# Performance work log

Hardware: AMD Instinct MI355X
Metric: run time of the kernel (lower is better)

The kernel has to match this reference:

```python
import jax, jax.numpy as jnp
import numpy as np


def setup_inputs() -> dict:
    key = jax.random.key(0)
    k1, k2 = jax.random.split(key)
    bz, c, h, w = 8, 512, 64, 64
    x = jax.random.normal(k1, (bz, c, h, w), dtype=jnp.float32)
    # binary mask over spatial positions; flag is its flattened view (must be consistent)
    mask = jax.random.randint(k2, (h, w), 0, 2, dtype=jnp.int32)
    flag = mask.reshape(-1)
    return {"input": x, "mask": mask, "flag": flag,
            "shift_sz": 1, "stride": 1, "triple_w": 1}


def reference(input, mask, flag, shift_sz, stride, triple_w):
    # input: [B, C, H, W]; former = first C/2 channels (decoder feats),
    # latter = last C/2 channels (encoder feats). shift_sz=stride=1 -> 1x1 patches,
    # i.e. per-pixel feature vectors.
    bz, c, h, w = input.shape
    ch = c // 2
    S = h * w
    former = input[:, :ch]                      # [B, ch, H, W]
    latter = input[:, ch:]                      # [B, ch, H, W]

    f = former.reshape(bz, ch, S).transpose(0, 2, 1)   # [B, S, ch] query pixels
    l = latter.reshape(bz, ch, S).transpose(0, 2, 1)   # [B, S, ch] key pixels

    # _norm: L2-normalize latter patches (rows)
    l_norm = l / jnp.maximum(jnp.linalg.norm(l, axis=-1, keepdims=True), 1e-12)

    # cosine-style similarity between every former pixel and every latter pixel
    sim = jnp.einsum('bqc,bkc->bqk', f, l_norm)        # [B, S, S]

    # only non-masked (flag==0) latter pixels are valid match candidates
    neg = jnp.asarray(-1e30, sim.dtype)
    sim = jnp.where((flag == 0)[None, None, :], sim, neg)
    idx = jnp.argmax(sim, axis=-1)                     # [B, S] nearest-neighbor index

    # gather matched latter pixels; paste only at masked (flag==1) positions,
    # zero elsewhere (masked_fill_(inv_ex_mask, 0) zeroes the non-mask region)
    shifted = jnp.take_along_axis(l, idx[..., None], axis=1)       # [B, S, ch]
    shifted = jnp.where((flag == 1)[None, :, None], shifted, 0.0)
    shifted = shifted.transpose(0, 2, 1).reshape(bz, ch, h, w)

    return jnp.concatenate([former, latter, shifted], axis=1)       # [B, 3*ch, H, W]
```

## Files before the change

### kernel.cpp

```cpp
#include <hip/hip_runtime.h>

#define S    4096
#define CH   256
#define NB   8

#define BM   64
#define BN   64
#define KSPLIT 8

#define SFF  256.0f
#define SLL  1024.0f

#define NEG_INF (-3.402823466e38f)

typedef _Float16 half8 __attribute__((ext_vector_type(8)));
typedef float    f32x4 __attribute__((ext_vector_type(4)));

__global__ void compact(const int* __restrict__ flag, int* __restrict__ cnts,
                        int* __restrict__ qlist, int* __restrict__ klist,
                        int* __restrict__ qpos,  int* __restrict__ kpos) {
    __shared__ int sq[256], sk[256];
    int t = threadIdx.x;
    int base = t * 16;
    int f[16];
    int nq = 0, nk = 0;
    #pragma unroll
    for (int i = 0; i < 16; ++i) {
        f[i] = flag[base + i];
        nq += (f[i] == 1);
        nk += (f[i] == 0);
    }
    sq[t] = nq; sk[t] = nk;
    __syncthreads();
    for (int off = 1; off < 256; off <<= 1) {
        int vq = sq[t], vk = sk[t];
        int aq = (t >= off) ? sq[t - off] : 0;
        int ak = (t >= off) ? sk[t - off] : 0;
        __syncthreads();
        sq[t] = vq + aq; sk[t] = vk + ak;
        __syncthreads();
    }
    int pq = sq[t] - nq;
    int pk = sk[t] - nk;
    #pragma unroll
    for (int i = 0; i < 16; ++i) {
        if (f[i] == 1) { qpos[base + i] = pq; qlist[pq++] = base + i; }
        else           { kpos[base + i] = pk; klist[pk++] = base + i; }
    }
    if (t == 255) { cnts[0] = sq[255]; cnts[1] = sk[255]; }
}

__global__ void pack_both(const float* __restrict__ x, const int* __restrict__ flag,
                          const int* __restrict__ qpos, const int* __restrict__ kpos,
                          float* __restrict__ out) {
    __shared__ float T[16][257];
    const int b = blockIdx.z;
    const int t = threadIdx.x;
    const int s = blockIdx.x * 256 + t;

    if (blockIdx.y < 4) {
        const int c0b = blockIdx.y * 64;
        const float* src = x + (size_t)b * 512 * S + blockIdx.x * 256;
        const bool active = (flag[s] == 1);
        const int row = active ? qpos[s] : 0;
        half8* F2 = (half8*)(out + (size_t)b * 768 * S);
        const int g  = row >> 4;
        const int sr = row & 15;
        for (int c0 = c0b; c0 < c0b + 64; c0 += 16) {
            #pragma unroll
            for (int i = 0; i < 16; ++i)
                T[i][t] = src[(size_t)(c0 + i) * S + t];
            __syncthreads();
            if (active) {
                #pragma unroll
                for (int g8 = 0; g8 < 2; ++g8) {
                    const int c  = c0 + g8 * 8;
                    const int cc = c >> 5;
                    const int l4 = (c >> 3) & 3;
                    half8 hb, lb;
                    #pragma unroll
                    for (int j = 0; j < 8; ++j) {
                        float v = T[g8 * 8 + j][t] * SFF;
                        _Float16 h = (_Float16)v;
                        hb[j] = h;
                        lb[j] = (_Float16)(v - (float)h);
                    }
                    F2[(size_t)(((g * 2 + 0) * 8 + cc) * 64) + sr * 4 + l4] = hb;
                    F2[(size_t)(((g * 2 + 1) * 8 + cc) * 64) + sr * 4 + l4] = lb;
                }
            }
            __syncthreads();
        }
    } else {
        const float* src = x + ((size_t)b * 512 + 256) * S + blockIdx.x * 256;
        const bool active = (flag[s] == 0);
        const int row = active ? kpos[s] : 0;
        _Float16* LH = (_Float16*)(out + (size_t)b * 768 * S) + 2 * (size_t)S * CH;
        _Float16* LL = LH + (size_t)S * CH;

        float acc = 0.f;
        for (int c0 = 0; c0 < CH; c0 += 16) {
            #pragma unroll
            for (int i = 0; i < 16; ++i)
                T[i][t] = src[(size_t)(c0 + i) * S + t];
            __syncthreads();
            #pragma unroll
            for (int i = 0; i < 16; ++i) {
                float v = T[i][t];
                acc += v * v;
            }
            __syncthreads();
        }
        const float w = active ? (1.0f / fmaxf(sqrtf(acc), 1e-12f)) * SLL : 0.f;

        for (int c0 = 0; c0 < CH; c0 += 16) {
            #pragma unroll
            for (int i = 0; i < 16; ++i)
                T[i][t] = src[(size_t)(c0 + i) * S + t];
            __syncthreads();
            if (active) {
                #pragma unroll
                for (int g8 = 0; g8 < 2; ++g8) {
                    union { _Float16 u[8]; float4 v; } hb, lb;
                    #pragma unroll
                    for (int j = 0; j < 8; ++j) {
                        float v = T[g8 * 8 + j][t] * w;
                        _Float16 h = (_Float16)v;
                        hb.u[j] = h;
                        lb.u[j] = (_Float16)(v - (float)h);
                    }
                    *(float4*)&LH[(size_t)row * CH + c0 + g8 * 8] = hb.v;
                    *(float4*)&LL[(size_t)row * CH + c0 + g8 * 8] = lb.v;
                }
            }
            __syncthreads();
        }
    }
}

__global__ void zero_pad(const int* __restrict__ cnts, float* __restrict__ out) {
    const int b  = blockIdx.y;
    const int Aq = cnts[0], Ak = cnts[1];
    const int aqp = (Aq + BM - 1) & ~(BM - 1);
    const int akp = (Ak + BN - 1) & ~(BN - 1);
    _Float16* pb = (_Float16*)(out + (size_t)b * 768 * S);
    int i = blockIdx.x * 256 + threadIdx.x;
    half8 z = { 0, 0, 0, 0, 0, 0, 0, 0 };
    if (i < 8192) {
        int p = i >> 12, rem = i & 4095;
        int row = Aq + (rem >> 5);
        int sl  = rem & 31;
        if (row < aqp) {
            half8* F2 = (half8*)pb;
            F2[(size_t)((((row >> 4) * 2 + p) * 8 + (sl >> 2)) * 64) + (row & 15) * 4 + (sl & 3)] = z;
        }
    } else {
        int j = i - 8192, panel = j >> 11, jdx = j & 2047;
        int row = Ak + (jdx >> 5);
        if (row < akp)
            *(half8*)(pb + (size_t)(2 + panel) * S * CH + (size_t)row * CH + (jdx & 31) * 8) = z;
    }
}

#define MFMA(A, B, C) __builtin_amdgcn_mfma_f32_16x16x32_f16((A), (B), (C), 0, 0, 0)

#define GLDS(SRC, OFF) __builtin_amdgcn_global_load_lds( \
    (const __attribute__((address_space(1))) void*)(SRC), \
    (__attribute__((address_space(3))) void*)(lds + (OFF)), 16, 0, 0)

#define STAGE(OFF) do { GLDS(s4, (OFF) + woff); GLDS(s5, (OFF) + 4096 + woff); } while (0)

#define ADV() do { \
    if (tn + 1 < nchunk) { \
        if ((tn & 7) == 7) { s4 += 32320; s5 += 32320; } \
        else               { s4 += 64;    s5 += 64;    } \
    } \
    ++tn; \
} while (0)

#define FOLD() do { \
    _Pragma("unroll") \
    for (int nt = 0; nt < 4; ++nt) { \
        int kp = kpb + nt * 16; \
        if (kp < Ak) { \
            _Pragma("unroll") \
            for (int r = 0; r < 4; ++r) { \
                float sv = acc[nt][r]; \
                if (sv > rm[r]) { rm[r] = sv; ri[r] = kp; } \
            } \
        } \
        acc[nt] = (f32x4){0.f, 0.f, 0.f, 0.f}; \
    } \
    kpb += 64; \
} while (0)

#define CBODY(BASE, CC) do { \
    const char* _bh = lds + (BASE) + boff0h; \
    const char* _bl = lds + (BASE) + boff0l; \
    half8 bh0 = *(const half8*)(_bh); \
    half8 bl0 = *(const half8*)(_bl); \
    half8 bh1 = *(const half8*)(_bh + 2048); \
    half8 bl1 = *(const half8*)(_bl + 2048); \
    half8 bh2 = *(const half8*)(_bh + 4096); \
    half8 bl2 = *(const half8*)(_bl + 4096); \
    half8 bh3 = *(const half8*)(_bh + 6144); \
    half8 bl3 = *(const half8*)(_bl + 6144); \
    acc[0] = MFMA(ah[CC], bh0, acc[0]); \
    acc[1] = MFMA(ah[CC], bh1, acc[1]); \
    acc[2] = MFMA(ah[CC], bh2, acc[2]); \
    acc[3] = MFMA(ah[CC], bh3, acc[3]); \
    acc[0] = MFMA(ah[CC], bl0, acc[0]); \
    acc[1] = MFMA(ah[CC], bl1, acc[1]); \
    acc[2] = MFMA(ah[CC], bl2, acc[2]); \
    acc[3] = MFMA(ah[CC], bl3, acc[3]); \
    acc[0] = MFMA(al[CC], bh0, acc[0]); \
    acc[1] = MFMA(al[CC], bh1, acc[1]); \
    acc[2] = MFMA(al[CC], bh2, acc[2]); \
    acc[3] = MFMA(al[CC], bh3, acc[3]); \
} while (0)

#define PHASE(J) do { \
    asm volatile("s_waitcnt vmcnt(4)" ::: "memory"); \
    __builtin_amdgcn_s_barrier(); \
    STAGE(sto); ADV(); \
    STAGE(sto + 8192); ADV(); \
    __builtin_amdgcn_s_setprio(1); \
    CBODY(rdo,        2 * (J)); \
    CBODY(rdo + 8192, 2 * (J) + 1); \
    __builtin_amdgcn_s_setprio(0); \
    rdo = (rdo == 32768) ? 0 : rdo + 16384; \
    sto = (sto == 32768) ? 0 : sto + 16384; \
} while (0)

__launch_bounds__(256)
__global__ void argmax_mfma(const float* __restrict__ outbuf,
                            const int*  __restrict__ cnts,
                            float* __restrict__ pmax,
                            int*   __restrict__ pidx) {
    __shared__ __align__(1024) char lds[6 * 8192];

    const int Aq    = cnts[0];
    const int Ak    = cnts[1];
    const int b     = blockIdx.y;
    const int split = blockIdx.x & (KSPLIT - 1);
    const int q0    = (blockIdx.x >> 3) * BM;
    if (q0 >= Aq) return;

    const int tid  = threadIdx.x;
    const int lane = tid & 63;
    const int wid  = tid >> 6;
    const int l15  = lane & 15;
    const int l4   = lane >> 4;
    const int woff = wid * 1024;

    const _Float16* pb  = (const _Float16*)(outbuf + (size_t)b * 768 * S);
    const _Float16* LHg = pb + 2 * (size_t)S * CH;
    const _Float16* LLg = pb + 3 * (size_t)S * CH;

    const int nkt = (Ak + BN - 1) / BN;
    const int kt0 = (nkt * split) / KSPLIT;
    const int kt1 = (nkt * (split + 1)) / KSPLIT;
    const int nchunk = (kt1 - kt0) * 8;

    float rm[4]; int ri[4];
    #pragma unroll
    for (int i = 0; i < 4; ++i) { rm[i] = NEG_INF; ri[i] = 0; }

    const int boff0h = l15 * 128 + ((l4 * 16) ^ ((l15 & 7) << 4));
    const int boff0l = boff0h ^ 64;

    if (nchunk > 0) {
        half8 ah[8], al[8];
        {
            const half8* F2 = (const half8*)pb;
            const int g0 = (q0 >> 4) + wid;
            const int lo = l15 * 4 + l4;
            #pragma unroll
            for (int cc = 0; cc < 8; ++cc) {
                ah[cc] = F2[(size_t)(((g0 * 2 + 0) * 8 + cc) * 64) + lo];
                al[cc] = F2[(size_t)(((g0 * 2 + 1) * 8 + cc) * 64) + lo];
            }
        }

        const char *s4, *s5;
        {
            #define LSRC(P) ({ int s_ = (P) * 256 + tid; int row_ = s_ >> 3; \
                int ls_ = (s_ & 7) ^ (row_ & 7); \
                (const char*)(((ls_ < 4) ? LHg : LLg) + (size_t)(kt0 * BN + row_) * CH + (ls_ & 3) * 8); })
            s4 = LSRC(0); s5 = LSRC(1);
            #undef LSRC
        }
        int tn = 0;

        f32x4 acc[4];
        #pragma unroll
        for (int nt = 0; nt < 4; ++nt) acc[nt] = (f32x4){0.f, 0.f, 0.f, 0.f};

        int kpb = kt0 * BN + l15;

        STAGE(0);     ADV();
        STAGE(8192);  ADV();
        STAGE(16384); ADV();
        STAGE(24576); ADV();

        int rdo = 0;
        int sto = 32768;
        const int ngroup = kt1 - kt0;
        for (int g = 0; g < ngroup; ++g) {
            PHASE(0);
            PHASE(1);
            PHASE(2);
            PHASE(3);
            FOLD();
        }
    }

    #pragma unroll
    for (int r = 0; r < 4; ++r) {
        float m = rm[r]; int id = ri[r];
        #pragma unroll
        for (int off = 8; off; off >>= 1) {
            float om = __shfl_xor(m, off, 64);
            int   oi = __shfl_xor(id, off, 64);
            if (om > m || (om == m && oi < id)) { m = om; id = oi; }
        }
        if (l15 == 0) {
            int qp = q0 + wid * 16 + l4 * 4 + r;
            if (qp < Aq) {
                size_t o = ((size_t)((b << 12) + qp)) * KSPLIT + split;
                pmax[o] = m;
                pidx[o] = id;
            }
        }
    }
}

__global__ void combine(const int* __restrict__ cnts, const int* __restrict__ qlist,
                        const int* __restrict__ klist,
                        const float* __restrict__ pmax, const int* __restrict__ pidx,
                        int* __restrict__ idxb) {
    int qp = blockIdx.x * 256 + threadIdx.x;
    int b  = blockIdx.y;
    if (qp >= cnts[0]) return;
    size_t base = (size_t)((b << 12) + qp) * KSPLIT;
    float m = pmax[base]; int id = pidx[base];
    #pragma unroll
    for (int s = 1; s < KSPLIT; ++s) {
        float om = pmax[base + s]; int oi = pidx[base + s];
        if (om > m) { m = om; id = oi; }
    }
    idxb[((size_t)b << 12) + qlist[qp]] = klist[id];
}

__global__ void writeback(const float* __restrict__ x, const int* __restrict__ flag,
                          const int* __restrict__ idxb, float* __restrict__ out) {
    int i = blockIdx.x * 256 + threadIdx.x;
    int b = blockIdx.y;
    int c = i >> 10;
    float4* dst = (float4*)(out + (size_t)b * 768 * S) + i;
    if (c < 512) {
        *dst = ((const float4*)(x + (size_t)b * 512 * S))[i];
    } else {
        const float* src = x + ((size_t)b * 512 + 256 + (c - 512)) * S;
        const int* ib = idxb + ((size_t)b << 12);
        int q = (i & 1023) * 4;
        float4 v = { 0.f, 0.f, 0.f, 0.f };
        if (flag[q + 0] == 1) v.x = src[ib[q + 0]];
        if (flag[q + 1] == 1) v.y = src[ib[q + 1]];
        if (flag[q + 2] == 1) v.z = src[ib[q + 2]];
        if (flag[q + 3] == 1) v.w = src[ib[q + 3]];
        *dst = v;
    }
}

extern "C" void kernel_launch(void* const* d_in, const int* in_sizes, int n_in,
                              void* d_out, int out_size, void* d_ws, size_t ws_size,
                              hipStream_t stream) {
    const float* x    = (const float*)d_in[0];
    const int*   flag = (const int*)d_in[2];
    float*       out  = (float*)d_out;

    char* ws = (char*)d_ws;
    int*   cnts  = (int*)(ws);
    int*   qlist = (int*)(ws + 1024);
    int*   klist = (int*)(ws + 17408);
    int*   qpos  = (int*)(ws + 33792);
    int*   kpos  = (int*)(ws + 50176);
    int*   idxb  = (int*)(ws + 66560);
    float* pmax  = (float*)(ws + 197632);
    int*   pidx  = (int*)(ws + 1246208);

    hipLaunchKernelGGL(compact,     dim3(1),                     dim3(256), 0, stream, flag, cnts, qlist, klist, qpos, kpos);
    hipLaunchKernelGGL(pack_both,   dim3(S / 256, 5, NB),        dim3(256), 0, stream, x, flag, qpos, kpos, out);
    hipLaunchKernelGGL(zero_pad,    dim3(48, NB),                dim3(256), 0, stream, cnts, out);
    hipLaunchKernelGGL(argmax_mfma, dim3((S / BM) * KSPLIT, NB), dim3(256), 0, stream, out, cnts, pmax, pidx);
    hipLaunchKernelGGL(combine,     dim3(S / 256, NB),           dim3(256), 0, stream, cnts, qlist, klist, pmax, pidx, idxb);
    hipLaunchKernelGGL(writeback,   dim3(768 * 1024 / 256, NB),  dim3(256), 0, stream, x, flag, idxb, out);
}
```

Before: 158.3 us.

## Restructure K-loop into a 4-buffer ring staging one chunk per barrier

Replaces the 6-slot LDS pipeline, which staged two chunks per phase with runtime-rotated read and write offsets, with a 4-slot ring. Each iteration stages one chunk and computes one, and all buffer offsets are compile-time constants across an 8-way unrolled loop. The running max is folded every 8 chunks. Less LDS per block may allow more resident blocks and removes offset arithmetic, at the cost of twice as many barriers, shallower prefetch depth, and an unchanged vmcnt(4) wait that may no longer match the load count.

```diff
diff --git a/kernel.cpp b/kernel.cpp
--- a/kernel.cpp
+++ b/kernel.cpp
@@ -219,17 +219,14 @@
     acc[3] = MFMA(al[CC], bh3, acc[3]); \
 } while (0)
 
-#define PHASE(J) do { \
+#define ITER(TL, BUFL, NXL) do { \
     asm volatile("s_waitcnt vmcnt(4)" ::: "memory"); \
     __builtin_amdgcn_s_barrier(); \
-    STAGE(sto); ADV(); \
-    STAGE(sto + 8192); ADV(); \
+    STAGE(NXL); ADV(); \
     __builtin_amdgcn_s_setprio(1); \
-    CBODY(rdo,        2 * (J)); \
-    CBODY(rdo + 8192, 2 * (J) + 1); \
+    CBODY(BUFL, TL); \
     __builtin_amdgcn_s_setprio(0); \
-    rdo = (rdo == 32768) ? 0 : rdo + 16384; \
-    sto = (sto == 32768) ? 0 : sto + 16384; \
+    if (((TL) & 7) == 7) FOLD(); \
 } while (0)
 
 __launch_bounds__(256)
@@ -237,7 +234,7 @@
                             const int*  __restrict__ cnts,
                             float* __restrict__ pmax,
                             int*   __restrict__ pidx) {
-    __shared__ __align__(1024) char lds[6 * 8192];
+    __shared__ __align__(1024) char lds[4 * 8192];
 
     const int Aq    = cnts[0];
     const int Ak    = cnts[1];
@@ -301,17 +298,16 @@
         STAGE(0);     ADV();
         STAGE(8192);  ADV();
         STAGE(16384); ADV();
-        STAGE(24576); ADV();
-
-        int rdo = 0;
-        int sto = 32768;
-        const int ngroup = kt1 - kt0;
-        for (int g = 0; g < ngroup; ++g) {
-            PHASE(0);
-            PHASE(1);
-            PHASE(2);
-            PHASE(3);
-            FOLD();
+
+        for (int t = 0; t < nchunk; t += 8) {
+            ITER(0, 0,     24576);
+            ITER(1, 8192,  0);
+            ITER(2, 16384, 8192);
+            ITER(3, 24576, 16384);
+            ITER(4, 0,     24576);
+            ITER(5, 8192,  0);
+            ITER(6, 16384, 8192);
+            ITER(7, 24576, 16384);
         }
     }
 
```

After: 158.1 us. About the same (-0.2%).
